# Kernel optimization log

Measured on AMD Instinct MI355X. Metric: run time of the kernel, lower is better.

## Reference

```python
import jax, jax.numpy as jnp
import numpy as np
import math

N = 100000
C = 128
E = 640000
ALPHA = 0.1
THETA = 1.0
LAYER = 4


def setup_inputs() -> dict:
    key = jax.random.key(0)
    k1, k2, k3, k4, k5, k6 = jax.random.split(key, 6)
    x = jax.random.normal(k1, (N, C), dtype=jnp.float32)
    x0 = jax.random.normal(k2, (N, C), dtype=jnp.float32)
    W = jax.random.normal(k3, (C, C), dtype=jnp.float32) / math.sqrt(C)
    b = jax.random.normal(k4, (C,), dtype=jnp.float32) * 0.01
    edge_index = jax.random.randint(k5, (2, E), 0, N, dtype=jnp.int64)
    return {"x": x, "x0": x0, "W": W, "b": b, "edge_index": edge_index}


def _symmetric_propagate(x, edge_index):
    n = x.shape[0]
    loop = jnp.arange(n, dtype=edge_index.dtype)
    src = jnp.concatenate([edge_index[0], loop])  # add self-loops (GCN norm)
    dst = jnp.concatenate([edge_index[1], loop])
    ones = jnp.ones(src.shape[0], dtype=x.dtype)
    deg = jax.ops.segment_sum(ones, dst, num_segments=n)
    dinv = jnp.where(deg > 0, jax.lax.rsqrt(deg), 0.0)
    norm = dinv[src] * dinv[dst]                  # [E+N]
    msgs = x[src] * norm[:, None]                 # gather + scale
    return jax.ops.segment_sum(msgs, dst, num_segments=n)  # scatter-add


def reference(x, x0, W, b, edge_index):
    propagated = _symmetric_propagate(x, edge_index)
    support = (1.0 - ALPHA) * propagated + ALPHA * x0
    beta = math.log(THETA / max(LAYER, 1) + 1.0)
    transformed = support @ W.T + b               # nn.Linear(channels, channels)
    return (1.0 - beta) * support + beta * transformed
```

## Files before the change

kernel.cpp:

```cpp
#include <hip/hip_runtime.h>
#include <stdint.h>

#define C 128
#define ALPHA_F 0.1f
#define ONE_MINUS_ALPHA 0.9f
#define BETA_F 0.22314355131420976f
#define ONE_MINUS_BETA 0.7768564486857902f

typedef __attribute__((ext_vector_type(8))) short bf16x8;
typedef __attribute__((ext_vector_type(4))) float f32x4;

__device__ inline float bf2f(unsigned short u) {
    union { unsigned int i; float f; } c;
    c.i = ((unsigned int)u) << 16;
    return c.f;
}
__device__ inline unsigned short f2bf(float f) {
    union { float f; unsigned int i; } c;
    c.f = f;
    unsigned int r = (c.i + 0x7FFFu + ((c.i >> 16) & 1u)) >> 16;
    return (unsigned short)r;
}

__global__ void k_init(const float* __restrict__ W, unsigned short* __restrict__ Vb,
                       int* __restrict__ cnt, int n) {
    int i = blockIdx.x * 256 + threadIdx.x;
    if (i < n) cnt[i] = 0;
    if (i < C * C) {
        int j = i >> 7;
        int c = i & 127;
        float v = BETA_F * W[i] + ((j == c) ? ONE_MINUS_BETA : 0.f);
        Vb[i] = f2bf(v);
    }
}

__global__ void k_hist(const int* __restrict__ dst, int* __restrict__ cnt,
                       int* __restrict__ rank, int e) {
    int i = blockIdx.x * blockDim.x + threadIdx.x;
    if (i < e) rank[i] = atomicAdd(&cnt[dst[i]], 1);
}

__global__ __launch_bounds__(256)
void k_scan_a(const int* __restrict__ cnt, int* __restrict__ part, int n) {
    __shared__ int s[256];
    int t = threadIdx.x;
    int i = blockIdx.x * 256 + t;
    s[t] = (i < n) ? cnt[i] : 0;
    __syncthreads();
    for (int off = 128; off > 0; off >>= 1) {
        if (t < off) s[t] += s[t + off];
        __syncthreads();
    }
    if (t == 0) part[blockIdx.x] = s[0];
}

__global__ __launch_bounds__(256)
void k_scan_bc(const int* __restrict__ cnt, const int* __restrict__ part,
               int4* __restrict__ meta, int* __restrict__ row_ptr,
               float* __restrict__ dinv, int n) {
    __shared__ int a[256];
    __shared__ int b[256];
    int t   = threadIdx.x;
    int bid = blockIdx.x;

    int local = 0;
    for (int k = t; k < bid; k += 256) local += part[k];
    a[t] = local;
    __syncthreads();
    for (int off = 128; off > 0; off >>= 1) {
        if (t < off) a[t] += a[t + off];
        __syncthreads();
    }
    int blockoff = a[0];
    __syncthreads();

    int i = bid * 256 + t;
    int v = (i < n) ? cnt[i] : 0;
    a[t] = v;
    __syncthreads();
    int* cur = a;
    int* nxt = b;
    for (int off = 1; off < 256; off <<= 1) {
        nxt[t] = cur[t] + ((t >= off) ? cur[t - off] : 0);
        __syncthreads();
        int* tmp = cur; cur = nxt; nxt = tmp;
    }
    if (i < n) {
        int rp = blockoff + cur[t] - v;
        float dv = rsqrtf((float)(v + 1));
        meta[i]    = make_int4(rp, v, __float_as_int(dv), 0);
        row_ptr[i] = rp;
        dinv[i]    = dv;
    }
}

__global__ void k_pl_ybf(const int* __restrict__ src, const int* __restrict__ dst,
                         const int* __restrict__ row_ptr, const int* __restrict__ rank,
                         int* __restrict__ sorted_src, int e,
                         const float* __restrict__ x, const float* __restrict__ dinv,
                         unsigned short* __restrict__ y, int n, int eb) {
    int bid = blockIdx.x;
    if (bid < eb) {
        int i = bid * 256 + threadIdx.x;
        if (i < e) {
            int d = dst[i];
            int pos = row_ptr[d] + rank[i];
            sorted_src[pos] = src[i];
        }
    } else {
        int t = (bid - eb) * 256 + threadIdx.x;
        int total = n * 32;
        if (t < total) {
            int i = t >> 5;
            float dv = dinv[i];
            float4 v = ((const float4*)x)[t];
            ushort4 o;
            o.x = f2bf(v.x * dv);
            o.y = f2bf(v.y * dv);
            o.z = f2bf(v.z * dv);
            o.w = f2bf(v.w * dv);
            ((ushort4*)y)[t] = o;
        }
    }
}

__device__ __forceinline__ float4 acc_node(const ushort4* __restrict__ y4,
                                           const int* __restrict__ ss,
                                           int node, int start, int len,
                                           int eidx, int l32, int base) {
    int m = (len < 32) ? len : 32;
    bool b1 = 1 < m, b2 = 2 < m, b3 = 3 < m;
    bool b4 = 4 < m, b5 = 5 < m, b6 = 6 < m, b7 = 7 < m;
    int s0 = __shfl(eidx, base + 0, 64);
    int s1 = __shfl(eidx, base + (b1 ? 1 : 0), 64);
    int s2 = __shfl(eidx, base + (b2 ? 2 : 0), 64);
    int s3 = __shfl(eidx, base + (b3 ? 3 : 0), 64);
    int s4 = __shfl(eidx, base + (b4 ? 4 : 0), 64);
    int s5 = __shfl(eidx, base + (b5 ? 5 : 0), 64);
    int s6 = __shfl(eidx, base + (b6 ? 6 : 0), 64);
    int s7 = __shfl(eidx, base + (b7 ? 7 : 0), 64);
    ushort4 v0 = y4[(size_t)s0 * 32 + l32];
    ushort4 v1 = y4[(size_t)s1 * 32 + l32];
    ushort4 v2 = y4[(size_t)s2 * 32 + l32];
    ushort4 v3 = y4[(size_t)s3 * 32 + l32];
    ushort4 v4 = y4[(size_t)s4 * 32 + l32];
    ushort4 v5 = y4[(size_t)s5 * 32 + l32];
    ushort4 v6 = y4[(size_t)s6 * 32 + l32];
    ushort4 v7 = y4[(size_t)s7 * 32 + l32];
    ushort4 vs = y4[(size_t)node * 32 + l32];

    float w0 = (0 < m) ? 1.f : 0.f, w1 = b1 ? 1.f : 0.f, w2 = b2 ? 1.f : 0.f, w3 = b3 ? 1.f : 0.f;
    float w4 = b4 ? 1.f : 0.f, w5 = b5 ? 1.f : 0.f, w6 = b6 ? 1.f : 0.f, w7 = b7 ? 1.f : 0.f;

    float4 acc;
    acc.x = bf2f(vs.x) + w0 * bf2f(v0.x) + w1 * bf2f(v1.x) + w2 * bf2f(v2.x) + w3 * bf2f(v3.x)
                       + w4 * bf2f(v4.x) + w5 * bf2f(v5.x) + w6 * bf2f(v6.x) + w7 * bf2f(v7.x);
    acc.y = bf2f(vs.y) + w0 * bf2f(v0.y) + w1 * bf2f(v1.y) + w2 * bf2f(v2.y) + w3 * bf2f(v3.y)
                       + w4 * bf2f(v4.y) + w5 * bf2f(v5.y) + w6 * bf2f(v6.y) + w7 * bf2f(v7.y);
    acc.z = bf2f(vs.z) + w0 * bf2f(v0.z) + w1 * bf2f(v1.z) + w2 * bf2f(v2.z) + w3 * bf2f(v3.z)
                       + w4 * bf2f(v4.z) + w5 * bf2f(v5.z) + w6 * bf2f(v6.z) + w7 * bf2f(v7.z);
    acc.w = bf2f(vs.w) + w0 * bf2f(v0.w) + w1 * bf2f(v1.w) + w2 * bf2f(v2.w) + w3 * bf2f(v3.w)
                       + w4 * bf2f(v4.w) + w5 * bf2f(v5.w) + w6 * bf2f(v6.w) + w7 * bf2f(v7.w);

    for (int j = 8; j < m; j += 4) {
        bool c1 = (j + 1) < m, c2 = (j + 2) < m, c3 = (j + 3) < m;
        int t0 = __shfl(eidx, base + j, 64);
        int t1 = __shfl(eidx, base + (c1 ? j + 1 : j), 64);
        int t2 = __shfl(eidx, base + (c2 ? j + 2 : j), 64);
        int t3 = __shfl(eidx, base + (c3 ? j + 3 : j), 64);
        ushort4 u0 = y4[(size_t)t0 * 32 + l32];
        ushort4 u1 = y4[(size_t)t1 * 32 + l32];
        ushort4 u2 = y4[(size_t)t2 * 32 + l32];
        ushort4 u3 = y4[(size_t)t3 * 32 + l32];
        float q1 = c1 ? 1.f : 0.f, q2 = c2 ? 1.f : 0.f, q3 = c3 ? 1.f : 0.f;
        acc.x += bf2f(u0.x) + q1 * bf2f(u1.x) + q2 * bf2f(u2.x) + q3 * bf2f(u3.x);
        acc.y += bf2f(u0.y) + q1 * bf2f(u1.y) + q2 * bf2f(u2.y) + q3 * bf2f(u3.y);
        acc.z += bf2f(u0.z) + q1 * bf2f(u1.z) + q2 * bf2f(u2.z) + q3 * bf2f(u3.z);
        acc.w += bf2f(u0.w) + q1 * bf2f(u1.w) + q2 * bf2f(u2.w) + q3 * bf2f(u3.w);
    }

    for (int j = 32; j < len; ++j) {
        int t0 = ss[start + j];
        ushort4 u0 = y4[(size_t)t0 * 32 + l32];
        acc.x += bf2f(u0.x);
        acc.y += bf2f(u0.y);
        acc.z += bf2f(u0.z);
        acc.w += bf2f(u0.w);
    }
    return acc;
}

__global__ __launch_bounds__(256)
void k_gather(const unsigned short* __restrict__ y, const float* __restrict__ x0,
              const int* __restrict__ sorted_src, const int4* __restrict__ meta,
              float* __restrict__ soutf, unsigned short* __restrict__ soutb,
              int mode, int n) {
    int tid  = threadIdx.x;
    int l32  = tid & 31;
    int base = tid & 32;
    int hw   = tid >> 5;
    int node0 = blockIdx.x * 16 + hw * 2;
    if (node0 >= n) return;
    int node1 = node0 + 1;
    bool ok1 = node1 < n;
    int vn1 = ok1 ? node1 : node0;

    const ushort4* y4 = (const ushort4*)y;
    const f32x4* x04 = (const f32x4*)x0;

    int4 md0 = meta[node0];
    int4 md1 = meta[vn1];
    int m0 = (md0.y < 32) ? md0.y : 32;
    int m1 = (md1.y < 32) ? md1.y : 32;
    int e0 = (l32 < m0) ? sorted_src[md0.x + l32] : node0;
    int e1 = (l32 < m1) ? sorted_src[md1.x + l32] : vn1;
    f32x4 xv0 = __builtin_nontemporal_load(x04 + (size_t)node0 * 32 + l32);
    f32x4 xv1 = __builtin_nontemporal_load(x04 + (size_t)vn1 * 32 + l32);

    float4 a0 = acc_node(y4, sorted_src, node0, md0.x, md0.y, e0, l32, base);
    float4 a1 = acc_node(y4, sorted_src, vn1,   md1.x, md1.y, e1, l32, base);

    float dv0 = __int_as_float(md0.z);
    float dv1 = __int_as_float(md1.z);

    float4 s0, s1;
    s0.x = ONE_MINUS_ALPHA * (dv0 * a0.x) + ALPHA_F * xv0.x;
    s0.y = ONE_MINUS_ALPHA * (dv0 * a0.y) + ALPHA_F * xv0.y;
    s0.z = ONE_MINUS_ALPHA * (dv0 * a0.z) + ALPHA_F * xv0.z;
    s0.w = ONE_MINUS_ALPHA * (dv0 * a0.w) + ALPHA_F * xv0.w;
    s1.x = ONE_MINUS_ALPHA * (dv1 * a1.x) + ALPHA_F * xv1.x;
    s1.y = ONE_MINUS_ALPHA * (dv1 * a1.y) + ALPHA_F * xv1.y;
    s1.z = ONE_MINUS_ALPHA * (dv1 * a1.z) + ALPHA_F * xv1.z;
    s1.w = ONE_MINUS_ALPHA * (dv1 * a1.w) + ALPHA_F * xv1.w;

    if (mode) {
        unsigned long long p0 =
            (unsigned long long)f2bf(s0.x)
          | ((unsigned long long)f2bf(s0.y) << 16)
          | ((unsigned long long)f2bf(s0.z) << 32)
          | ((unsigned long long)f2bf(s0.w) << 48);
        __builtin_nontemporal_store(
            p0, (unsigned long long*)(soutb + (size_t)node0 * C + l32 * 4));
        if (ok1) {
            unsigned long long p1 =
                (unsigned long long)f2bf(s1.x)
              | ((unsigned long long)f2bf(s1.y) << 16)
              | ((unsigned long long)f2bf(s1.z) << 32)
              | ((unsigned long long)f2bf(s1.w) << 48);
            __builtin_nontemporal_store(
                p1, (unsigned long long*)(soutb + (size_t)node1 * C + l32 * 4));
        }
    } else {
        ((float4*)soutf)[(size_t)node0 * 32 + l32] = s0;
        if (ok1) ((float4*)soutf)[(size_t)node1 * 32 + l32] = s1;
    }
}

__global__ __launch_bounds__(256)
void k_out(const float* __restrict__ sinf, const unsigned short* __restrict__ sinb,
           const unsigned short* __restrict__ Vb, const float* __restrict__ bias,
           float* __restrict__ out, int mode, int n) {
    __shared__ unsigned short wlds[128 * 128];
    __shared__ unsigned short slds[64 * 128];

    int tid  = threadIdx.x;
    int row0 = blockIdx.x * 64;

    const uint4* Vb16 = (const uint4*)Vb;
    for (int i = tid; i < 2048; i += 256) {
        int j = i >> 4;
        int g = i & 15;
        uint4 v = Vb16[i];
        *(uint4*)&wlds[j * 128 + (g ^ (j & 7)) * 8] = v;
    }

    if (mode) {
        const uint4* sb16 = (const uint4*)sinb;
        for (int i = tid; i < 1024; i += 256) {
            int r = i >> 4;
            int g = i & 15;
            int grow = row0 + r;
            uint4 v = make_uint4(0, 0, 0, 0);
            if (grow < n) v = sb16[(size_t)grow * 16 + g];
            *(uint4*)&slds[r * 128 + (g ^ (r & 7)) * 8] = v;
        }
    } else {
        for (int i = tid; i < 1024; i += 256) {
            int r = i >> 4;
            int g = i & 15;
            int grow = row0 + r;
            union { unsigned short u[8]; uint4 v; } pk;
            if (grow < n) {
                const float* p = sinf + (size_t)grow * C + g * 8;
                float4 aa = *(const float4*)p;
                float4 bb = *(const float4*)(p + 4);
                pk.u[0] = f2bf(aa.x); pk.u[1] = f2bf(aa.y);
                pk.u[2] = f2bf(aa.z); pk.u[3] = f2bf(aa.w);
                pk.u[4] = f2bf(bb.x); pk.u[5] = f2bf(bb.y);
                pk.u[6] = f2bf(bb.z); pk.u[7] = f2bf(bb.w);
            } else {
                pk.v = make_uint4(0, 0, 0, 0);
            }
            *(uint4*)&slds[r * 128 + (g ^ (r & 7)) * 8] = pk.v;
        }
    }
    __syncthreads();

    int w    = tid >> 6;
    int lane = tid & 63;
    int l16  = lane & 15;
    int h    = lane >> 4;
    int arow = w * 16 + l16;

    f32x4 acc[8];
    #pragma unroll
    for (int t = 0; t < 8; ++t) acc[t] = (f32x4){0.f, 0.f, 0.f, 0.f};

    #pragma unroll
    for (int k0 = 0; k0 < 128; k0 += 32) {
        int ga = ((k0 >> 3) + h) ^ (arow & 7);
        bf16x8 a = *(const bf16x8*)&slds[arow * 128 + ga * 8];
        #pragma unroll
        for (int t = 0; t < 8; ++t) {
            int brow = t * 16 + l16;
            int gb = ((k0 >> 3) + h) ^ (brow & 7);
            bf16x8 b = *(const bf16x8*)&wlds[brow * 128 + gb * 8];
            acc[t] = __builtin_amdgcn_mfma_f32_16x16x32_bf16(a, b, acc[t], 0, 0, 0);
        }
    }

    #pragma unroll
    for (int t = 0; t < 8; ++t) {
        int j  = t * 16 + l16;
        float bj = BETA_F * bias[j];
        #pragma unroll
        for (int e2 = 0; e2 < 4; ++e2) {
            int grow = row0 + w * 16 + h * 4 + e2;
            if (grow < n) {
                __builtin_nontemporal_store(acc[t][e2] + bj, &out[(size_t)grow * C + j]);
            }
        }
    }
}

extern "C" void kernel_launch(void* const* d_in, const int* in_sizes, int n_in,
                              void* d_out, int out_size, void* d_ws, size_t ws_size,
                              hipStream_t stream) {
    const float* x   = (const float*)d_in[0];
    const float* x0  = (const float*)d_in[1];
    const float* W   = (const float*)d_in[2];
    const float* b   = (const float*)d_in[3];
    const int*   ei  = (const int*)d_in[4];

    int n = in_sizes[0] / C;
    int e = in_sizes[4] / 2;
    const int* src = ei;
    const int* dst = ei + e;

    int*   cnt        = (int*)d_ws;
    float* dinv       = (float*)(cnt + n);
    int*   part       = (int*)(dinv + n);
    int4*  meta       = (int4*)(part + 512);
    int*   row_ptr    = (int*)(meta + n);
    int*   rank       = row_ptr + n;
    int*   sorted_src = rank + e;
    unsigned short* Vb   = (unsigned short*)(sorted_src + e);
    unsigned short* y    = Vb + C * C;
    unsigned short* sb16 = y + (size_t)n * C;

    size_t need = (size_t)((char*)(sb16 + (size_t)n * C) - (char*)d_ws);
    int mode = (ws_size >= need) ? 1 : 0;

    float* out = (float*)d_out;

    int nb  = (n + 255) / 256;
    int eb  = (e + 255) / 256;
    int ybg = (n * 32 + 255) / 256;

    k_init   <<<nb, 256, 0, stream>>>(W, Vb, cnt, n);
    k_hist   <<<eb, 256, 0, stream>>>(dst, cnt, rank, e);
    k_scan_a <<<nb, 256, 0, stream>>>(cnt, part, n);
    k_scan_bc<<<nb, 256, 0, stream>>>(cnt, part, meta, row_ptr, dinv, n);
    k_pl_ybf <<<eb + ybg, 256, 0, stream>>>(src, dst, row_ptr, rank, sorted_src, e,
                                            x, dinv, y, n, eb);
    k_gather <<<(n + 15) / 16, 256, 0, stream>>>(y, x0, sorted_src, meta,
                                                 out, sb16, mode, n);
    k_out    <<<(n + 63) / 64, 256, 0, stream>>>(out, sb16, Vb, b, out, mode, n);
}
```

Baseline: 127.2 us.

## Merge CSR preprocessing kernels into one cooperative kernel with grid syncs

Replaces five separate preprocessing launches (init, histogram, two scan phases, placement plus bf16 scaling) with a single cooperative kernel of 1024 blocks that uses grid-stride loops and grid.sync between phases. The aim is to remove per-launch overhead and inter-kernel gaps. In exchange it adds grid-wide barrier cost, and the smaller fixed grid may lower parallelism in the bandwidth-bound phases. The cooperative launch also needs all 1024 blocks to be resident at once.

```diff
diff --git a/kernel.cpp b/kernel.cpp
--- a/kernel.cpp
+++ b/kernel.cpp
@@ -1,5 +1,8 @@
 #include <hip/hip_runtime.h>
+#include <hip/hip_cooperative_groups.h>
 #include <stdint.h>
+
+namespace cg = cooperative_groups;
 
 #define C 128
 #define ALPHA_F 0.1f
@@ -22,105 +25,97 @@
     return (unsigned short)r;
 }
 
-__global__ void k_init(const float* __restrict__ W, unsigned short* __restrict__ Vb,
-                       int* __restrict__ cnt, int n) {
-    int i = blockIdx.x * 256 + threadIdx.x;
-    if (i < n) cnt[i] = 0;
-    if (i < C * C) {
+__global__ __launch_bounds__(256)
+void k_pre(const float* __restrict__ W, unsigned short* __restrict__ Vb,
+           int* __restrict__ cnt, int* __restrict__ rank,
+           const int* __restrict__ src, const int* __restrict__ dst,
+           int* __restrict__ row_ptr, int4* __restrict__ meta,
+           float* __restrict__ dinv, int* __restrict__ part,
+           int* __restrict__ sorted_src,
+           const float* __restrict__ x, unsigned short* __restrict__ y,
+           int n, int e, int nb) {
+    cg::grid_group grid = cg::this_grid();
+    __shared__ int sa[256];
+    __shared__ int sb[256];
+
+    int tid     = threadIdx.x;
+    int gsz     = gridDim.x;
+    int gtid    = blockIdx.x * 256 + tid;
+    int gstride = gsz * 256;
+
+    for (int i = gtid; i < n; i += gstride) cnt[i] = 0;
+    for (int i = gtid; i < C * C; i += gstride) {
         int j = i >> 7;
         int c = i & 127;
-        float v = BETA_F * W[i] + ((j == c) ? ONE_MINUS_BETA : 0.f);
-        Vb[i] = f2bf(v);
-    }
-}
-
-__global__ void k_hist(const int* __restrict__ dst, int* __restrict__ cnt,
-                       int* __restrict__ rank, int e) {
-    int i = blockIdx.x * blockDim.x + threadIdx.x;
-    if (i < e) rank[i] = atomicAdd(&cnt[dst[i]], 1);
-}
-
-__global__ __launch_bounds__(256)
-void k_scan_a(const int* __restrict__ cnt, int* __restrict__ part, int n) {
-    __shared__ int s[256];
-    int t = threadIdx.x;
-    int i = blockIdx.x * 256 + t;
-    s[t] = (i < n) ? cnt[i] : 0;
-    __syncthreads();
-    for (int off = 128; off > 0; off >>= 1) {
-        if (t < off) s[t] += s[t + off];
-        __syncthreads();
-    }
-    if (t == 0) part[blockIdx.x] = s[0];
-}
-
-__global__ __launch_bounds__(256)
-void k_scan_bc(const int* __restrict__ cnt, const int* __restrict__ part,
-               int4* __restrict__ meta, int* __restrict__ row_ptr,
-               float* __restrict__ dinv, int n) {
-    __shared__ int a[256];
-    __shared__ int b[256];
-    int t   = threadIdx.x;
-    int bid = blockIdx.x;
-
-    int local = 0;
-    for (int k = t; k < bid; k += 256) local += part[k];
-    a[t] = local;
-    __syncthreads();
-    for (int off = 128; off > 0; off >>= 1) {
-        if (t < off) a[t] += a[t + off];
-        __syncthreads();
-    }
-    int blockoff = a[0];
-    __syncthreads();
-
-    int i = bid * 256 + t;
-    int v = (i < n) ? cnt[i] : 0;
-    a[t] = v;
-    __syncthreads();
-    int* cur = a;
-    int* nxt = b;
-    for (int off = 1; off < 256; off <<= 1) {
-        nxt[t] = cur[t] + ((t >= off) ? cur[t - off] : 0);
-        __syncthreads();
-        int* tmp = cur; cur = nxt; nxt = tmp;
-    }
-    if (i < n) {
-        int rp = blockoff + cur[t] - v;
-        float dv = rsqrtf((float)(v + 1));
-        meta[i]    = make_int4(rp, v, __float_as_int(dv), 0);
-        row_ptr[i] = rp;
-        dinv[i]    = dv;
-    }
-}
-
-__global__ void k_pl_ybf(const int* __restrict__ src, const int* __restrict__ dst,
-                         const int* __restrict__ row_ptr, const int* __restrict__ rank,
-                         int* __restrict__ sorted_src, int e,
-                         const float* __restrict__ x, const float* __restrict__ dinv,
-                         unsigned short* __restrict__ y, int n, int eb) {
-    int bid = blockIdx.x;
-    if (bid < eb) {
-        int i = bid * 256 + threadIdx.x;
-        if (i < e) {
-            int d = dst[i];
-            int pos = row_ptr[d] + rank[i];
-            sorted_src[pos] = src[i];
-        }
-    } else {
-        int t = (bid - eb) * 256 + threadIdx.x;
-        int total = n * 32;
-        if (t < total) {
-            int i = t >> 5;
-            float dv = dinv[i];
-            float4 v = ((const float4*)x)[t];
-            ushort4 o;
-            o.x = f2bf(v.x * dv);
-            o.y = f2bf(v.y * dv);
-            o.z = f2bf(v.z * dv);
-            o.w = f2bf(v.w * dv);
-            ((ushort4*)y)[t] = o;
-        }
+        Vb[i] = f2bf(BETA_F * W[i] + ((j == c) ? ONE_MINUS_BETA : 0.f));
+    }
+    grid.sync();
+
+    for (int i = gtid; i < e; i += gstride) rank[i] = atomicAdd(&cnt[dst[i]], 1);
+    grid.sync();
+
+    for (int vb = blockIdx.x; vb < nb; vb += gsz) {
+        int i = vb * 256 + tid;
+        sa[tid] = (i < n) ? cnt[i] : 0;
+        __syncthreads();
+        for (int off = 128; off > 0; off >>= 1) {
+            if (tid < off) sa[tid] += sa[tid + off];
+            __syncthreads();
+        }
+        if (tid == 0) part[vb] = sa[0];
+        __syncthreads();
+    }
+    grid.sync();
+
+    for (int vb = blockIdx.x; vb < nb; vb += gsz) {
+        int local = 0;
+        for (int k = tid; k < vb; k += 256) local += part[k];
+        sa[tid] = local;
+        __syncthreads();
+        for (int off = 128; off > 0; off >>= 1) {
+            if (tid < off) sa[tid] += sa[tid + off];
+            __syncthreads();
+        }
+        int blockoff = sa[0];
+        __syncthreads();
+
+        int i = vb * 256 + tid;
+        int v = (i < n) ? cnt[i] : 0;
+        sa[tid] = v;
+        __syncthreads();
+        int* cur = sa;
+        int* nxt = sb;
+        for (int off = 1; off < 256; off <<= 1) {
+            nxt[tid] = cur[tid] + ((tid >= off) ? cur[tid - off] : 0);
+            __syncthreads();
+            int* tmp = cur; cur = nxt; nxt = tmp;
+        }
+        if (i < n) {
+            int rp = blockoff + cur[tid] - v;
+            float dv = rsqrtf((float)(v + 1));
+            meta[i]    = make_int4(rp, v, __float_as_int(dv), 0);
+            row_ptr[i] = rp;
+            dinv[i]    = dv;
+        }
+        __syncthreads();
+    }
+    grid.sync();
+
+    for (int i = gtid; i < e; i += gstride) {
+        int d = dst[i];
+        sorted_src[row_ptr[d] + rank[i]] = src[i];
+    }
+    int total = n * 32;
+    for (int t = gtid; t < total; t += gstride) {
+        int i = t >> 5;
+        float dv = dinv[i];
+        float4 v = ((const float4*)x)[t];
+        ushort4 o;
+        o.x = f2bf(v.x * dv);
+        o.y = f2bf(v.y * dv);
+        o.z = f2bf(v.z * dv);
+        o.w = f2bf(v.w * dv);
+        ((ushort4*)y)[t] = o;
     }
 }
 
@@ -373,17 +368,19 @@
 
     float* out = (float*)d_out;
 
-    int nb  = (n + 255) / 256;
-    int eb  = (e + 255) / 256;
-    int ybg = (n * 32 + 255) / 256;
-
-    k_init   <<<nb, 256, 0, stream>>>(W, Vb, cnt, n);
-    k_hist   <<<eb, 256, 0, stream>>>(dst, cnt, rank, e);
-    k_scan_a <<<nb, 256, 0, stream>>>(cnt, part, n);
-    k_scan_bc<<<nb, 256, 0, stream>>>(cnt, part, meta, row_ptr, dinv, n);
-    k_pl_ybf <<<eb + ybg, 256, 0, stream>>>(src, dst, row_ptr, rank, sorted_src, e,
-                                            x, dinv, y, n, eb);
-    k_gather <<<(n + 15) / 16, 256, 0, stream>>>(y, x0, sorted_src, meta,
-                                                 out, sb16, mode, n);
-    k_out    <<<(n + 63) / 64, 256, 0, stream>>>(out, sb16, Vb, b, out, mode, n);
-}
+    int nb = (n + 255) / 256;
+
+    {
+        void* args[] = {
+            (void*)&W, (void*)&Vb, (void*)&cnt, (void*)&rank,
+            (void*)&src, (void*)&dst, (void*)&row_ptr, (void*)&meta,
+            (void*)&dinv, (void*)&part, (void*)&sorted_src,
+            (void*)&x, (void*)&y, (void*)&n, (void*)&e, (void*)&nb
+        };
+        hipLaunchCooperativeKernel((const void*)k_pre, dim3(1024), dim3(256),
+                                   args, 0, stream);
+    }
+    k_gather<<<(n + 15) / 16, 256, 0, stream>>>(y, x0, sorted_src, meta,
+                                                out, sb16, mode, n);
+    k_out   <<<(n + 63) / 64, 256, 0, stream>>>(out, sb16, Vb, b, out, mode, n);
+}
```

Measured after the change: 508.4 us. 300% more time.
